# Kernel tuning notes

Measured on AMD Instinct MI355X. Metric: run time of the kernel, lower is better.

## Reference

```python
import jax, jax.numpy as jnp
import numpy as np

N = 50000      # nodes
E = 800000     # edges (no self-loops; conv adds them)
EMB = 64       # emb_dim
H = 4          # heads
C = EMB // H   # out_channels per head
L = 3          # num_layer
NEG = 0.2      # leaky_relu negative slope
EPS = 1e-5     # batchnorm eps


def setup_inputs() -> dict:
    key = jax.random.key(0)
    ks = jax.random.split(key, 12)
    x_idx = jax.random.randint(ks[0], (N,), 0, 16)
    src = jax.random.randint(ks[1], (E,), 0, N)
    off = jax.random.randint(ks[2], (E,), 1, N)
    dst = (src + off) % N  # guaranteed no self-loops
    edge_index = jnp.stack([src, dst])
    edge_attr_idx = jax.random.randint(ks[3], (E,), 0, 4)
    s = 0.1
    atom_emb = jax.random.normal(ks[4], (16, EMB)) * s
    W = jax.random.normal(ks[5], (L, EMB, H * C)) * s          # lin_src == lin_dst (shared)
    att_src = jax.random.normal(ks[6], (L, H, C)) * s
    att_dst = jax.random.normal(ks[7], (L, H, C)) * s
    att_edge = jax.random.normal(ks[8], (L, H, C)) * s
    bias = jnp.zeros((L, H * C))
    edge_emb = jax.random.normal(ks[9], (L, 4, H * C)) * s     # lin_edge embedding per layer
    bn_gamma = jnp.ones((L, EMB))
    bn_beta = jnp.zeros((L, EMB))
    pred_W = jax.random.normal(ks[10], (2 * EMB, 1)) * s
    pred_b = jnp.zeros((1,))
    return dict(x_idx=x_idx, edge_index=edge_index, edge_attr_idx=edge_attr_idx,
                atom_emb=atom_emb, W=W, att_src=att_src, att_dst=att_dst,
                att_edge=att_edge, bias=bias, edge_emb=edge_emb,
                bn_gamma=bn_gamma, bn_beta=bn_beta, pred_W=pred_W, pred_b=pred_b)


def _gat_forward(x_idx, edge_index, edge_attr_idx, atom_emb, W, att_src, att_dst,
                 att_edge, bias, edge_emb, bn_gamma, bn_beta, pred_W, pred_b):
    src, dst = edge_index[0], edge_index[1]
    loop = jnp.arange(N)
    src2 = jnp.concatenate([src, loop])   # edges + self-loops
    dst2 = jnp.concatenate([dst, loop])
    x = atom_emb[x_idx]                   # [N, EMB]
    for l in range(L):
        # embed edge attrs, self-loop fill = mean of incoming-edge features per node
        ea = edge_emb[l][edge_attr_idx]                                   # [E, H*C]
        cnt = jax.ops.segment_sum(jnp.ones((E,), ea.dtype), dst, N)       # [N]
        ea_mean = jax.ops.segment_sum(ea, dst, N) / jnp.clip(cnt, 1.0)[:, None]
        ea2 = jnp.concatenate([ea, ea_mean]).reshape(-1, H, C)            # [E+N, H, C]
        # shared src/dst projection
        xl = (x @ W[l]).reshape(N, H, C)                                  # [N, H, C]
        a_src = jnp.sum(xl * att_src[l], axis=-1)                         # [N, H]
        a_dst = jnp.sum(xl * att_dst[l], axis=-1)                         # [N, H]
        a_edge = jnp.sum(ea2 * att_edge[l], axis=-1)                      # [E+N, H]
        alpha = a_src[src2] + a_dst[dst2] + a_edge
        alpha = jnp.where(alpha >= 0, alpha, NEG * alpha)                 # leaky_relu
        # segment softmax over incoming edges of each destination node
        m = jax.ops.segment_max(alpha, dst2, N)                           # [N, H]
        ex = jnp.exp(alpha - m[dst2])
        denom = jax.ops.segment_sum(ex, dst2, N)
        alpha = ex / denom[dst2]                                          # [E+N, H]
        # message + scatter-add aggregate
        msg = alpha[:, :, None] * (xl[src2] + ea2)                        # [E+N, H, C]
        out = jax.ops.segment_sum(msg, dst2, N).reshape(N, H * C) + bias[l]
        # BatchNorm1d (training-mode batch stats, biased variance)
        mu = jnp.mean(out, axis=0)
        var = jnp.mean((out - mu) ** 2, axis=0)
        out = (out - mu) * jax.lax.rsqrt(var + EPS) * bn_gamma[l] + bn_beta[l]
        x = jax.nn.relu(out) + x                                          # residual
    pair = jnp.concatenate([x[src], x[dst]], axis=-1)                     # [E, 2*EMB]
    return pair @ pred_W + pred_b                                         # [E, 1]


def reference(x_idx, edge_index, edge_attr_idx, atom_emb, W, att_src, att_dst,
              att_edge, bias, edge_emb, bn_gamma, bn_beta, pred_W, pred_b):
    return _gat_forward(x_idx, edge_index, edge_attr_idx, atom_emb, W, att_src,
                        att_dst, att_edge, bias, edge_emb, bn_gamma, bn_beta,
                        pred_W, pred_b)
```

## Files before the change

kernel.cpp:

```cpp
#include <hip/hip_runtime.h>
#include <hip/hip_bf16.h>

#define NN 50000
#define NE 800000
#define NEG 0.2f
#define BNEPS 1e-5f
#define NB_CVT 61
#define NB_EDGE 3125
#define NB1 200
#define CH1 4000
#define NBKT 250
#define CAPBKT 4096
#define MAXS 288
#define NPARTS 32
#define NB_FRONT (NB_CVT + 1 + NB1)
#define NB_MID (NBKT + NN/16)

typedef __hip_bfloat16 bf16;
typedef unsigned short u16;
typedef unsigned int u32;
__device__ __forceinline__ float b2f(bf16 v){ return __bfloat162float(v); }
__device__ __forceinline__ float u2f(u16 u){ return __uint_as_float(((u32)u) << 16); }
__device__ __forceinline__ u16 f2u(float f){ bf16 b = __float2bfloat16(f); return *(u16*)&b; }

struct CvtArgs { const void* src[11]; int off[11]; int cnt[11]; };

__global__ __launch_bounds__(256) void k_front(CvtArgs a, const void* eeraw,
        const void* aeraw, const int* __restrict__ src, const int* __restrict__ dst,
        const int* __restrict__ ety,
        float* __restrict__ cw, float* __restrict__ aet, int* __restrict__ flag,
        int* __restrict__ bcur, u32* __restrict__ bins){
  int t = threadIdx.x, b = blockIdx.x;
  if (b >= NB_CVT + 1){
    __shared__ int cnt[NBKT], start[NBKT], cur[NBKT];
    __shared__ int dcache[CH1];
    int bb = b - (NB_CVT + 1);
    for (int i = t; i < NBKT; i += 256){ cnt[i] = 0; cur[i] = 0; }
    __syncthreads();
    int base = bb*CH1;
    for (int k = t; k < CH1; k += 256){
      int d = dst[base + k];
      dcache[k] = d;
      atomicAdd(&cnt[(u32)d/200u], 1);
    }
    __syncthreads();
    for (int i = t; i < NBKT; i += 256) start[i] = atomicAdd(&bcur[i], cnt[i]);
    __syncthreads();
    for (int k = t; k < CH1; k += 256){
      int e = base + k;
      u32 d = (u32)dcache[k];
      u32 bk = d/200u;
      int pos = start[bk] + atomicAdd(&cur[bk], 1);
      if (pos < CAPBKT)
        bins[bk*CAPBKT + pos] = (u32)src[e] | ((u32)ety[e] << 16) | ((d - bk*200u) << 18);
    }
    return;
  }
  __shared__ int sflag;
  if (t < 64){
    const u16* u = (const u16*)a.src[0];
    int hit = 0;
    for (int i = t; i < 512; i += 64){
      int ex = (u[i] >> 7) & 0xFF;
      if (ex >= 0x8A || (ex != 0 && ex <= 0x60)) hit = 1;
    }
    unsigned long long bl = __ballot(hit);
    if (t == 0) sflag = (bl != 0ULL) ? 1 : 0;
  }
  __syncthreads();
  int f = sflag;
  if (b == 0 && t == 0) *flag = f;
  if (b < NB_CVT){
    int i = b*256 + t;
    #pragma unroll
    for (int s = 0; s < 11; ++s){
      int j = i - a.off[s];
      if (j >= 0 && j < a.cnt[s])
        cw[a.off[s] + j] = f ? ((const float*)a.src[s])[j]
                             : b2f(((const bf16*)a.src[s])[j]);
    }
  } else if (t < 48){
    int l = t >> 4, ty = (t >> 2) & 3, h = t & 3;
    float s = 0.f;
    for (int cc = 0; cc < 16; ++cc){
      int ei = l*256 + ty*64 + h*16 + cc;
      int ai = l*64 + h*16 + cc;
      float ev = f ? ((const float*)eeraw)[ei] : b2f(((const bf16*)eeraw)[ei]);
      float av = f ? ((const float*)aeraw)[ai] : b2f(((const bf16*)aeraw)[ai]);
      s += ev*av;
    }
    aet[t] = s;
  }
}

__global__ __launch_bounds__(256) void k_mid(const int* __restrict__ bcur,
        const u32* __restrict__ bins,
        int* __restrict__ cpack, int* __restrict__ rowst, int* __restrict__ cnt4,
        const int* __restrict__ xidx, const float* __restrict__ aembf,
        const float* __restrict__ Wl, const float* __restrict__ att_s,
        const float* __restrict__ att_d,
        float* __restrict__ x, u16* __restrict__ bxl,
        float* __restrict__ asrc, float* __restrict__ adst){
  __shared__ __align__(16) char smem[17408];
  int t = threadIdx.x, b = blockIdx.x;
  if (b < NBKT){
    int* c4   = (int*)smem;
    int* nst  = c4 + 800;
    int* ncur = nst + 200;
    int* bco  = ncur + 200;
    int* s    = bco + 256;
    for (int i = t; i < 800; i += 256) c4[i] = 0;
    if (t < 200) ncur[t] = 0;
    int v = 0;
    if (t < NBKT){ v = bcur[t]; if (v > CAPBKT) v = CAPBKT; }
    bco[t] = v; s[t] = v;
    __syncthreads();
    for (int o = 1; o < 256; o <<= 1){
      int a2 = s[t]; int add = (t >= o) ? s[t-o] : 0;
      __syncthreads(); s[t] = a2 + add; __syncthreads();
    }
    int gb = s[b] - bco[b];
    int tot = bco[b];
    int total = s[255];
    __syncthreads();
    for (int i = t; i < tot; i += 256){
      u32 e = bins[b*CAPBKT + i];
      atomicAdd(&c4[((e >> 18) & 0xFF)*4 + ((e >> 16) & 3)], 1);
    }
    __syncthreads();
    int deg = 0;
    if (t < 200) deg = c4[t*4] + c4[t*4+1] + c4[t*4+2] + c4[t*4+3];
    s[t] = deg; __syncthreads();
    for (int o = 1; o < 256; o <<= 1){
      int a2 = s[t]; int add = (t >= o) ? s[t-o] : 0;
      __syncthreads(); s[t] = a2 + add; __syncthreads();
    }
    if (t < 200) nst[t] = s[t] - deg;
    __syncthreads();
    if (t < 200){
      int n = b*200 + t;
      rowst[n] = gb + nst[t];
      *(int4*)&cnt4[n*4] = make_int4(c4[t*4], c4[t*4+1], c4[t*4+2], c4[t*4+3]);
    }
    if (b == 0 && t == 0) rowst[NN] = total;
    for (int i = t; i < tot; i += 256){
      u32 e = bins[b*CAPBKT + i];
      int nl = (e >> 18) & 0xFF;
      int pos = nst[nl] + atomicAdd(&ncur[nl], 1);
      cpack[gb + pos] = (int)(e & 0x3FFFF);
    }
    return;
  }
  float* Ws = (float*)smem;
  float* xs = Ws + 4096;
  int bp = b - NBKT;
  for (int i = t; i < 4096; i += 256) Ws[i] = Wl[i];
  int c = t & 63, wv = t >> 6;
  float ats = att_s[c], atd = att_d[c];
  for (int pass = 0; pass < 4; ++pass){
    int n = bp*16 + pass*4 + wv;
    float xv = aembf[xidx[n]*64 + c];
    x[n*64 + c] = xv;
    __syncthreads();
    xs[t] = xv;
    __syncthreads();
    const float* xr = &xs[wv*64];
    float acc = 0.f;
    #pragma unroll
    for (int k = 0; k < 64; ++k) acc += xr[k]*Ws[k*64 + c];
    bxl[n*64 + c] = f2u(acc);
    float vs = acc*ats, vd = acc*atd;
    #pragma unroll
    for (int o = 8; o >= 1; o >>= 1){ vs += __shfl_xor(vs,o,64); vd += __shfl_xor(vd,o,64); }
    if ((c & 15) == 0){ asrc[n*4 + (c>>4)] = vs; adst[n*4 + (c>>4)] = vd; }
  }
}

__global__ __launch_bounds__(256) void k_bnproj(
    const float* __restrict__ opre, const float* __restrict__ bnp,
    const float* __restrict__ gam, const float* __restrict__ bet,
    const float* __restrict__ Wl,
    const float* __restrict__ att_s, const float* __restrict__ att_d,
    float* __restrict__ x, u16* __restrict__ bxl,
    float* __restrict__ asrc, float* __restrict__ adst){
  __shared__ float Ws[4096];
  __shared__ float xs[256];
  __shared__ float sred[256];
  __shared__ float stat[128];
  int t = threadIdx.x;
  {
    int cc = t & 127;
    float s = 0.f;
    for (int p2 = t >> 7; p2 < NPARTS; p2 += 2) s += bnp[p2*128 + cc];
    sred[t] = s;
  }
  for (int i = t; i < 4096; i += 256) Ws[i] = Wl[i];
  __syncthreads();
  if (t < 128) stat[t] = sred[t] + sred[128 + t];
  __syncthreads();
  int c = t & 63, wv = t >> 6;
  float mu  = stat[c] * (1.f/NN);
  float var = stat[64+c] * (1.f/NN) - mu*mu;
  float rstd = rsqrtf(var + BNEPS);
  float g = gam[c], be = bet[c];
  float ats = att_s[c], atd = att_d[c];
  for (int pass = 0; pass < 4; ++pass){
    int n = blockIdx.x*16 + pass*4 + wv;
    float o = (opre[n*64 + c] - mu)*rstd*g + be;
    float xv = x[n*64 + c] + fmaxf(o, 0.f);
    x[n*64 + c] = xv;
    __syncthreads();
    xs[t] = xv;
    __syncthreads();
    const float* xr = &xs[wv*64];
    float acc = 0.f;
    #pragma unroll
    for (int k = 0; k < 64; ++k) acc += xr[k]*Ws[k*64 + c];
    bxl[n*64 + c] = f2u(acc);
    float vs = acc*ats, vd = acc*atd;
    #pragma unroll
    for (int o2 = 8; o2 >= 1; o2 >>= 1){ vs += __shfl_xor(vs,o2,64); vd += __shfl_xor(vd,o2,64); }
    if ((c & 15) == 0){ asrc[n*4 + (c>>4)] = vs; adst[n*4 + (c>>4)] = vd; }
  }
}

__global__ __launch_bounds__(256) void k_aggr(
    const u16* __restrict__ bxl,
    const float* __restrict__ asrc, const float* __restrict__ adst,
    const int* __restrict__ cnt4, const int* __restrict__ rowst,
    const int* __restrict__ cpack,
    const float* __restrict__ eeg, const float* __restrict__ aetg,
    const float* __restrict__ biasg,
    float* __restrict__ opre, float* __restrict__ bnp){
  __shared__ __align__(16) float ee[256];
  __shared__ float aetL[16];
  __shared__ float adl[32];
  __shared__ float4 wsh[MAXS];
  __shared__ int ents[MAXS];
  __shared__ float redA[256], redB[256];
  __shared__ int rs[9];
  int t = threadIdx.x;
  int n0 = blockIdx.x*8;
  ee[t] = eeg[t];
  if (t < 16) aetL[t] = aetg[t];
  if (t >= 32 && t < 64) adl[t-32] = adst[n0*4 + (t-32)];
  if (t >= 64 && t < 73) rs[t-64] = rowst[n0 + (t-64)];
  __syncthreads();
  int jb0 = rs[0], je0 = rs[8], cnt = je0 - jb0;
  int lim = cnt < MAXS ? cnt : MAXS;
  for (int s = t; s < lim; s += 256){
    int j = jb0 + s;
    int pk = cpack[j];
    ents[s] = pk;
    int sr = pk & 0xFFFF, ty = pk >> 16;
    int dl = (j>=rs[1])+(j>=rs[2])+(j>=rs[3])+(j>=rs[4])+(j>=rs[5])+(j>=rs[6])+(j>=rs[7]);
    float4 as4 = *(const float4*)&asrc[sr*4];
    float a0 = as4.x + adl[dl*4+0] + aetL[ty*4+0]; a0 = a0>=0.f ? a0 : NEG*a0;
    float a1 = as4.y + adl[dl*4+1] + aetL[ty*4+1]; a1 = a1>=0.f ? a1 : NEG*a1;
    float a2 = as4.z + adl[dl*4+2] + aetL[ty*4+2]; a2 = a2>=0.f ? a2 : NEG*a2;
    float a3 = as4.w + adl[dl*4+3] + aetL[ty*4+3]; a3 = a3>=0.f ? a3 : NEG*a3;
    wsh[s] = make_float4(__expf(a0), __expf(a1), __expf(a2), __expf(a3));
  }
  __syncthreads();
  int wv = t >> 6, lane = t & 63;
  int ep = lane >> 5;
  int li = lane & 31;
  int ci = li << 1;
  int h = ci >> 4;
  const u32* bxl32 = (const u32*)bxl;
  const float* wshf = (const float*)wsh;
  float sA0 = 0.f, sA1 = 0.f, sB0 = 0.f, sB1 = 0.f;
  #pragma unroll
  for (int half = 0; half < 2; ++half){
    int node = wv + half*4;
    int n = n0 + node;
    int jb = rs[node], je = rs[node+1];
    int4 c4 = *(const int4*)&cnt4[n*4];
    int deg = c4.x + c4.y + c4.z + c4.w;
    float inv = 1.f / (float)(deg > 0 ? deg : 1);
    float2 eA = *(const float2*)&ee[ci];
    float2 eB = *(const float2*)&ee[64+ci];
    float2 eC = *(const float2*)&ee[128+ci];
    float2 eD = *(const float2*)&ee[192+ci];
    float eam0 = ((float)c4.x*eA.x + (float)c4.y*eB.x + (float)c4.z*eC.x + (float)c4.w*eD.x)*inv;
    float eam1 = ((float)c4.x*eA.y + (float)c4.y*eB.y + (float)c4.z*eC.y + (float)c4.w*eD.y)*inv;
    float aes = ((float)c4.x*aetL[h] + (float)c4.y*aetL[4+h]
               + (float)c4.z*aetL[8+h] + (float)c4.w*aetL[12+h]) * inv;
    float adn = adl[node*4 + h];
    float a = asrc[n*4 + h] + adn + aes;
    a = a >= 0.f ? a : NEG*a;
    float wself = __expf(a);
    u32 vs_ = bxl32[n*32 + li];
    float acc0, acc1, den;
    if (ep == 0){
      den = wself;
      acc0 = wself*(__uint_as_float(vs_ << 16) + eam0);
      acc1 = wself*(__uint_as_float(vs_ & 0xFFFF0000u) + eam1);
    } else { den = 0.f; acc0 = 0.f; acc1 = 0.f; }
    int jlim = jb0 + lim;
    int jeP = je < jlim ? je : jlim;
    int j = jb;
    for (; j + 8 <= jeP; j += 8){
      int so = j - jb0 + ep;
      int p0 = ents[so], p1 = ents[so+2], p2 = ents[so+4], p3 = ents[so+6];
      u32 v0 = bxl32[(p0 & 0xFFFF)*32 + li];
      u32 v1 = bxl32[(p1 & 0xFFFF)*32 + li];
      u32 v2 = bxl32[(p2 & 0xFFFF)*32 + li];
      u32 v3 = bxl32[(p3 & 0xFFFF)*32 + li];
      float w0 = wshf[(so  )*4 + h], w1 = wshf[(so+2)*4 + h];
      float w2 = wshf[(so+4)*4 + h], w3 = wshf[(so+6)*4 + h];
      float2 e0 = *(const float2*)&ee[(p0 >> 16)*64 + ci];
      float2 e1 = *(const float2*)&ee[(p1 >> 16)*64 + ci];
      float2 e2 = *(const float2*)&ee[(p2 >> 16)*64 + ci];
      float2 e3 = *(const float2*)&ee[(p3 >> 16)*64 + ci];
      acc0 += w0*(__uint_as_float(v0 << 16) + e0.x);
      acc1 += w0*(__uint_as_float(v0 & 0xFFFF0000u) + e0.y); den += w0;
      acc0 += w1*(__uint_as_float(v1 << 16) + e1.x);
      acc1 += w1*(__uint_as_float(v1 & 0xFFFF0000u) + e1.y); den += w1;
      acc0 += w2*(__uint_as_float(v2 << 16) + e2.x);
      acc1 += w2*(__uint_as_float(v2 & 0xFFFF0000u) + e2.y); den += w2;
      acc0 += w3*(__uint_as_float(v3 << 16) + e3.x);
      acc1 += w3*(__uint_as_float(v3 & 0xFFFF0000u) + e3.y); den += w3;
    }
    for (; j + 2 <= jeP; j += 2){
      int so = j - jb0 + ep;
      int p = ents[so];
      u32 v = bxl32[(p & 0xFFFF)*32 + li];
      float w = wshf[so*4 + h];
      float2 e = *(const float2*)&ee[(p >> 16)*64 + ci];
      acc0 += w*(__uint_as_float(v << 16) + e.x);
      acc1 += w*(__uint_as_float(v & 0xFFFF0000u) + e.y);
      den += w;
    }
    if (j < jeP && ep == 0){
      int so = j - jb0;
      int p = ents[so];
      u32 v = bxl32[(p & 0xFFFF)*32 + li];
      float w = wshf[so*4 + h];
      float2 e = *(const float2*)&ee[(p >> 16)*64 + ci];
      acc0 += w*(__uint_as_float(v << 16) + e.x);
      acc1 += w*(__uint_as_float(v & 0xFFFF0000u) + e.y);
      den += w;
    }
    for (j = jeP; j < je; ++j){
      if (ep == 0){
        int pk = cpack[j];
        int s_ = pk & 0xFFFF, ty = pk >> 16;
        float aa = asrc[s_*4 + h] + adn + aetL[ty*4 + h];
        aa = aa >= 0.f ? aa : NEG*aa;
        float wj = __expf(aa);
        u32 v = bxl32[s_*32 + li];
        float2 e = *(const float2*)&ee[ty*64 + ci];
        acc0 += wj*(__uint_as_float(v << 16) + e.x);
        acc1 += wj*(__uint_as_float(v & 0xFFFF0000u) + e.y);
        den += wj;
      }
    }
    acc0 += __shfl_xor(acc0, 32, 64);
    acc1 += __shfl_xor(acc1, 32, 64);
    den  += __shfl_xor(den, 32, 64);
    float2 bi = *(const float2*)&biasg[ci];
    float out0 = acc0/den + bi.x;
    float out1 = acc1/den + bi.y;
    if (ep == 0) *(float2*)&opre[n*64 + ci] = make_float2(out0, out1);
    sA0 += out0; sA1 += out1; sB0 += out0*out0; sB1 += out1*out1;
  }
  if (ep == 0){
    redA[wv*64 + ci] = sA0; redA[wv*64 + ci + 1] = sA1;
    redB[wv*64 + ci] = sB0; redB[wv*64 + ci + 1] = sB1;
  }
  __syncthreads();
  int part = blockIdx.x & (NPARTS-1);
  if (t < 64){
    atomicAdd(&bnp[part*128 + t], redA[t]+redA[64+t]+redA[128+t]+redA[192+t]);
  } else if (t < 128){
    int cc = t - 64;
    atomicAdd(&bnp[part*128 + 64 + cc], redB[cc]+redB[64+cc]+redB[128+cc]+redB[192+cc]);
  }
}

__global__ __launch_bounds__(256) void k_bnpred(
    const float* __restrict__ x, const float* __restrict__ opre,
    const float* __restrict__ bnp, const float* __restrict__ gam,
    const float* __restrict__ bet, const float* __restrict__ pW,
    float* __restrict__ s1, float* __restrict__ s2){
  __shared__ float sred[256];
  __shared__ float stat[128];
  int t = threadIdx.x;
  {
    int cc = t & 127;
    float s = 0.f;
    for (int p2 = t >> 7; p2 < NPARTS; p2 += 2) s += bnp[p2*128 + cc];
    sred[t] = s;
  }
  __syncthreads();
  if (t < 128) stat[t] = sred[t] + sred[128 + t];
  __syncthreads();
  int wv = t >> 6, c = t & 63;
  int n = blockIdx.x*4 + wv;
  float mu  = stat[c] * (1.f/NN);
  float var = stat[64+c] * (1.f/NN) - mu*mu;
  float o = (opre[n*64 + c] - mu)*rsqrtf(var + BNEPS)*gam[c] + bet[c];
  float xv = x[n*64 + c] + fmaxf(o, 0.f);
  float v1 = xv*pW[c], v2 = xv*pW[64 + c];
  #pragma unroll
  for (int o2 = 32; o2 >= 1; o2 >>= 1){ v1 += __shfl_xor(v1,o2,64); v2 += __shfl_xor(v2,o2,64); }
  if (c == 0){ s1[n] = v1; s2[n] = v2; }
}

__global__ void k_pred_edge(const int* __restrict__ src, const int* __restrict__ dst,
        const float* __restrict__ s1, const float* __restrict__ s2,
        const float* __restrict__ pbf, const int* __restrict__ flag, void* out){
  int e = blockIdx.x*256 + threadIdx.x;
  if (e < NE){
    float v = s1[src[e]] + s2[dst[e]] + pbf[0];
    if (*flag) ((float*)out)[e] = v;
    else       ((bf16*)out)[e] = __float2bfloat16(v);
  }
}

extern "C" void kernel_launch(void* const* d_in, const int* in_sizes, int n_in,
                              void* d_out, int out_size, void* d_ws, size_t ws_size,
                              hipStream_t stream){
  const int*  xidx = (const int*)d_in[0];
  const int*  eidx = (const int*)d_in[1];
  const int*  ety  = (const int*)d_in[2];
  const int* srcp = eidx, *dstp = eidx + NE;

  char* base = (char*)d_ws;
  auto alloc = [&](size_t bytes) -> char* {
    char* r = base; base += (bytes + 255) & ~(size_t)255; return r;
  };
  float* x      = (float*)alloc(NN*64*4);
  float* opre   = (float*)alloc(NN*64*4);
  float* asrc   = (float*)alloc(NN*4*4);
  float* adst   = (float*)alloc(NN*4*4);
  float* s1     = (float*)alloc(NN*4);
  float* s2     = (float*)alloc(NN*4);
  float* cw     = (float*)alloc(15392*4);
  float* aet    = (float*)alloc(64*4);
  char*  zchunk = alloc(3*NPARTS*128*4 + 256*4);
  float* bnpart = (float*)zchunk;
  int*   bcur   = (int*)(zchunk + 3*NPARTS*128*4);
  size_t zbytes = 3*NPARTS*128*4 + 256*4;
  u32*   bins   = (u32*)alloc((size_t)NBKT*CAPBKT*4);
  int*   cpack  = (int*)alloc(NE*4);
  int*   rowst  = (int*)alloc((NN+4)*4);
  int*   cnt4   = (int*)alloc(NN*4*4);
  int*   flag   = (int*)alloc(256);
  u16*   bxl    = (u16*)alloc(NN*64*2);

  const int O_AEMB = 0,     N_AEMB = 1024;
  const int O_W    = 1024,  N_W    = 12288;
  const int O_AS   = 13312, N_AS   = 192;
  const int O_AD   = 13504, N_AD   = 192;
  const int O_AE   = 13696, N_AE   = 192;
  const int O_BI   = 13888, N_BI   = 192;
  const int O_EE   = 14080, N_EE   = 768;
  const int O_GA   = 14848, N_GA   = 192;
  const int O_BE   = 15040, N_BE   = 192;
  const int O_PW   = 15232, N_PW   = 128;
  const int O_PB   = 15360, N_PB   = 1;

  CvtArgs ca;
  ca.src[0]=d_in[3];  ca.off[0]=O_AEMB; ca.cnt[0]=N_AEMB;
  ca.src[1]=d_in[4];  ca.off[1]=O_W;    ca.cnt[1]=N_W;
  ca.src[2]=d_in[5];  ca.off[2]=O_AS;   ca.cnt[2]=N_AS;
  ca.src[3]=d_in[6];  ca.off[3]=O_AD;   ca.cnt[3]=N_AD;
  ca.src[4]=d_in[7];  ca.off[4]=O_AE;   ca.cnt[4]=N_AE;
  ca.src[5]=d_in[8];  ca.off[5]=O_BI;   ca.cnt[5]=N_BI;
  ca.src[6]=d_in[9];  ca.off[6]=O_EE;   ca.cnt[6]=N_EE;
  ca.src[7]=d_in[10]; ca.off[7]=O_GA;   ca.cnt[7]=N_GA;
  ca.src[8]=d_in[11]; ca.off[8]=O_BE;   ca.cnt[8]=N_BE;
  ca.src[9]=d_in[12]; ca.off[9]=O_PW;   ca.cnt[9]=N_PW;
  ca.src[10]=d_in[13];ca.off[10]=O_PB;  ca.cnt[10]=N_PB;

  hipMemsetAsync(zchunk, 0, zbytes, stream);
  k_front<<<NB_FRONT, 256, 0, stream>>>(ca, d_in[9], d_in[7], srcp, dstp, ety,
                                        cw, aet, flag, bcur, bins);
  k_mid<<<NB_MID, 256, 0, stream>>>(bcur, bins, cpack, rowst, cnt4,
                                    xidx, cw + O_AEMB, cw + O_W,
                                    cw + O_AS, cw + O_AD, x, bxl, asrc, adst);
  for (int l = 0; l < 3; ++l){
    k_aggr<<<NN/8, 256, 0, stream>>>(bxl, asrc, adst, cnt4, rowst, cpack,
                                     cw + O_EE + l*256, aet + l*16,
                                     cw + O_BI + l*64, opre, bnpart + l*NPARTS*128);
    if (l < 2)
      k_bnproj<<<NN/16, 256, 0, stream>>>(opre, bnpart + l*NPARTS*128,
                                          cw + O_GA + l*64, cw + O_BE + l*64,
                                          cw + O_W + (l+1)*4096,
                                          cw + O_AS + (l+1)*64, cw + O_AD + (l+1)*64,
                                          x, bxl, asrc, adst);
  }
  k_bnpred<<<NN/4, 256, 0, stream>>>(x, opre, bnpart + 2*NPARTS*128,
                                     cw + O_GA + 128, cw + O_BE + 128,
                                     cw + O_PW, s1, s2);
  k_pred_edge<<<NB_EDGE, 256, 0, stream>>>(srcp, dstp, s1, s2, cw + O_PB, flag, d_out);
}
```

Before: 248.5 us.

## Factor edge-embedding term out of aggregation loop via per-type weight sums

The attention weights of the edges cached in shared memory are now accumulated per (destination node, edge type, head) with shared-memory atomics. Each node's edge-embedding contribution and softmax denominator are then formed once from these sums instead of per edge. The source index and a bf16-rounded weight are packed into one u32 per head, so the inner loop does one LDS load and drops the edge-embedding and denominator work. This cuts shared-memory traffic and ALU per edge, at the cost of bf16 rounding of the attention weights and extra LDS atomics in the setup phase.

```diff
diff --git a/kernel.cpp b/kernel.cpp
--- a/kernel.cpp
+++ b/kernel.cpp
@@ -235,8 +235,8 @@
   __shared__ __align__(16) float ee[256];
   __shared__ float aetL[16];
   __shared__ float adl[32];
-  __shared__ float4 wsh[MAXS];
-  __shared__ int ents[MAXS];
+  __shared__ u32 wsl[4*MAXS];
+  __shared__ float wsum[128];
   __shared__ float redA[256], redB[256];
   __shared__ int rs[9];
   int t = threadIdx.x;
@@ -245,13 +245,13 @@
   if (t < 16) aetL[t] = aetg[t];
   if (t >= 32 && t < 64) adl[t-32] = adst[n0*4 + (t-32)];
   if (t >= 64 && t < 73) rs[t-64] = rowst[n0 + (t-64)];
-  __syncthreads();
-  int jb0 = rs[0], je0 = rs[8], cnt = je0 - jb0;
+  if (t >= 128) wsum[t-128] = 0.f;
+  __syncthreads();
+  int jb0 = rs[0], cnt = rs[8] - jb0;
   int lim = cnt < MAXS ? cnt : MAXS;
   for (int s = t; s < lim; s += 256){
     int j = jb0 + s;
     int pk = cpack[j];
-    ents[s] = pk;
     int sr = pk & 0xFFFF, ty = pk >> 16;
     int dl = (j>=rs[1])+(j>=rs[2])+(j>=rs[3])+(j>=rs[4])+(j>=rs[5])+(j>=rs[6])+(j>=rs[7]);
     float4 as4 = *(const float4*)&asrc[sr*4];
@@ -259,16 +259,25 @@
     float a1 = as4.y + adl[dl*4+1] + aetL[ty*4+1]; a1 = a1>=0.f ? a1 : NEG*a1;
     float a2 = as4.z + adl[dl*4+2] + aetL[ty*4+2]; a2 = a2>=0.f ? a2 : NEG*a2;
     float a3 = as4.w + adl[dl*4+3] + aetL[ty*4+3]; a3 = a3>=0.f ? a3 : NEG*a3;
-    wsh[s] = make_float4(__expf(a0), __expf(a1), __expf(a2), __expf(a3));
+    u32 sr16 = (u32)sr << 16;
+    u16 b0 = f2u(__expf(a0)), b1 = f2u(__expf(a1));
+    u16 b2 = f2u(__expf(a2)), b3 = f2u(__expf(a3));
+    wsl[s]        = sr16 | b0;
+    wsl[MAXS+s]   = sr16 | b1;
+    wsl[2*MAXS+s] = sr16 | b2;
+    wsl[3*MAXS+s] = sr16 | b3;
+    int wb = dl*16 + ty*4;
+    atomicAdd(&wsum[wb+0], u2f(b0));
+    atomicAdd(&wsum[wb+1], u2f(b1));
+    atomicAdd(&wsum[wb+2], u2f(b2));
+    atomicAdd(&wsum[wb+3], u2f(b3));
   }
   __syncthreads();
   int wv = t >> 6, lane = t & 63;
-  int ep = lane >> 5;
-  int li = lane & 31;
-  int ci = li << 1;
-  int h = ci >> 4;
+  int ep = lane >> 5, li = lane & 31;
+  int ci = li << 1, h = ci >> 4;
   const u32* bxl32 = (const u32*)bxl;
-  const float* wshf = (const float*)wsh;
+  const u32* whp = &wsl[h*MAXS];
   float sA0 = 0.f, sA1 = 0.f, sB0 = 0.f, sB1 = 0.f;
   #pragma unroll
   for (int half = 0; half < 2; ++half){
@@ -282,67 +291,62 @@
     float2 eB = *(const float2*)&ee[64+ci];
     float2 eC = *(const float2*)&ee[128+ci];
     float2 eD = *(const float2*)&ee[192+ci];
-    float eam0 = ((float)c4.x*eA.x + (float)c4.y*eB.x + (float)c4.z*eC.x + (float)c4.w*eD.x)*inv;
-    float eam1 = ((float)c4.x*eA.y + (float)c4.y*eB.y + (float)c4.z*eC.y + (float)c4.w*eD.y)*inv;
     float aes = ((float)c4.x*aetL[h] + (float)c4.y*aetL[4+h]
                + (float)c4.z*aetL[8+h] + (float)c4.w*aetL[12+h]) * inv;
     float adn = adl[node*4 + h];
     float a = asrc[n*4 + h] + adn + aes;
     a = a >= 0.f ? a : NEG*a;
     float wself = __expf(a);
-    u32 vs_ = bxl32[n*32 + li];
-    float acc0, acc1, den;
+    float acc0 = 0.f, acc1 = 0.f, den = 0.f;
     if (ep == 0){
-      den = wself;
-      acc0 = wself*(__uint_as_float(vs_ << 16) + eam0);
-      acc1 = wself*(__uint_as_float(vs_ & 0xFFFF0000u) + eam1);
-    } else { den = 0.f; acc0 = 0.f; acc1 = 0.f; }
+      float eam0 = ((float)c4.x*eA.x + (float)c4.y*eB.x + (float)c4.z*eC.x + (float)c4.w*eD.x)*inv;
+      float eam1 = ((float)c4.x*eA.y + (float)c4.y*eB.y + (float)c4.z*eC.y + (float)c4.w*eD.y)*inv;
+      u32 vs_ = bxl32[n*32 + li];
+      float s0 = wsum[node*16 + h],     s1w = wsum[node*16 + 4 + h];
+      float s2w = wsum[node*16 + 8 + h], s3w = wsum[node*16 + 12 + h];
+      den = wself + s0 + s1w + s2w + s3w;
+      acc0 = wself*(__uint_as_float(vs_ << 16) + eam0)
+           + s0*eA.x + s1w*eB.x + s2w*eC.x + s3w*eD.x;
+      acc1 = wself*(__uint_as_float(vs_ & 0xFFFF0000u) + eam1)
+           + s0*eA.y + s1w*eB.y + s2w*eC.y + s3w*eD.y;
+    }
     int jlim = jb0 + lim;
     int jeP = je < jlim ? je : jlim;
     int j = jb;
     for (; j + 8 <= jeP; j += 8){
       int so = j - jb0 + ep;
-      int p0 = ents[so], p1 = ents[so+2], p2 = ents[so+4], p3 = ents[so+6];
-      u32 v0 = bxl32[(p0 & 0xFFFF)*32 + li];
-      u32 v1 = bxl32[(p1 & 0xFFFF)*32 + li];
-      u32 v2 = bxl32[(p2 & 0xFFFF)*32 + li];
-      u32 v3 = bxl32[(p3 & 0xFFFF)*32 + li];
-      float w0 = wshf[(so  )*4 + h], w1 = wshf[(so+2)*4 + h];
-      float w2 = wshf[(so+4)*4 + h], w3 = wshf[(so+6)*4 + h];
-      float2 e0 = *(const float2*)&ee[(p0 >> 16)*64 + ci];
-      float2 e1 = *(const float2*)&ee[(p1 >> 16)*64 + ci];
-      float2 e2 = *(const float2*)&ee[(p2 >> 16)*64 + ci];
-      float2 e3 = *(const float2*)&ee[(p3 >> 16)*64 + ci];
-      acc0 += w0*(__uint_as_float(v0 << 16) + e0.x);
-      acc1 += w0*(__uint_as_float(v0 & 0xFFFF0000u) + e0.y); den += w0;
-      acc0 += w1*(__uint_as_float(v1 << 16) + e1.x);
-      acc1 += w1*(__uint_as_float(v1 & 0xFFFF0000u) + e1.y); den += w1;
-      acc0 += w2*(__uint_as_float(v2 << 16) + e2.x);
-      acc1 += w2*(__uint_as_float(v2 & 0xFFFF0000u) + e2.y); den += w2;
-      acc0 += w3*(__uint_as_float(v3 << 16) + e3.x);
-      acc1 += w3*(__uint_as_float(v3 & 0xFFFF0000u) + e3.y); den += w3;
+      u32 p0 = whp[so],   p1 = whp[so+2], p2 = whp[so+4], p3 = whp[so+6];
+      u32 v0 = bxl32[(p0>>16)*32 + li], v1 = bxl32[(p1>>16)*32 + li];
+      u32 v2 = bxl32[(p2>>16)*32 + li], v3 = bxl32[(p3>>16)*32 + li];
+      float w0 = __uint_as_float(p0 << 16), w1 = __uint_as_float(p1 << 16);
+      float w2 = __uint_as_float(p2 << 16), w3 = __uint_as_float(p3 << 16);
+      acc0 += w0*__uint_as_float(v0 << 16);
+      acc1 += w0*__uint_as_float(v0 & 0xFFFF0000u);
+      acc0 += w1*__uint_as_float(v1 << 16);
+      acc1 += w1*__uint_as_float(v1 & 0xFFFF0000u);
+      acc0 += w2*__uint_as_float(v2 << 16);
+      acc1 += w2*__uint_as_float(v2 & 0xFFFF0000u);
+      acc0 += w3*__uint_as_float(v3 << 16);
+      acc1 += w3*__uint_as_float(v3 & 0xFFFF0000u);
     }
     for (; j + 2 <= jeP; j += 2){
       int so = j - jb0 + ep;
-      int p = ents[so];
-      u32 v = bxl32[(p & 0xFFFF)*32 + li];
-      float w = wshf[so*4 + h];
-      float2 e = *(const float2*)&ee[(p >> 16)*64 + ci];
-      acc0 += w*(__uint_as_float(v << 16) + e.x);
-      acc1 += w*(__uint_as_float(v & 0xFFFF0000u) + e.y);
-      den += w;
+      u32 p = whp[so];
+      u32 v = bxl32[(p>>16)*32 + li];
+      float w = __uint_as_float(p << 16);
+      acc0 += w*__uint_as_float(v << 16);
+      acc1 += w*__uint_as_float(v & 0xFFFF0000u);
     }
     if (j < jeP && ep == 0){
       int so = j - jb0;
-      int p = ents[so];
-      u32 v = bxl32[(p & 0xFFFF)*32 + li];
-      float w = wshf[so*4 + h];
-      float2 e = *(const float2*)&ee[(p >> 16)*64 + ci];
-      acc0 += w*(__uint_as_float(v << 16) + e.x);
-      acc1 += w*(__uint_as_float(v & 0xFFFF0000u) + e.y);
-      den += w;
-    }
-    for (j = jeP; j < je; ++j){
+      u32 p = whp[so];
+      u32 v = bxl32[(p>>16)*32 + li];
+      float w = __uint_as_float(p << 16);
+      acc0 += w*__uint_as_float(v << 16);
+      acc1 += w*__uint_as_float(v & 0xFFFF0000u);
+    }
+    int jf = jeP > jb ? jeP : jb;
+    for (j = jf; j < je; ++j){
       if (ep == 0){
         int pk = cpack[j];
         int s_ = pk & 0xFFFF, ty = pk >> 16;
@@ -358,12 +362,13 @@
     }
     acc0 += __shfl_xor(acc0, 32, 64);
     acc1 += __shfl_xor(acc1, 32, 64);
-    den  += __shfl_xor(den, 32, 64);
-    float2 bi = *(const float2*)&biasg[ci];
-    float out0 = acc0/den + bi.x;
-    float out1 = acc1/den + bi.y;
-    if (ep == 0) *(float2*)&opre[n*64 + ci] = make_float2(out0, out1);
-    sA0 += out0; sA1 += out1; sB0 += out0*out0; sB1 += out1*out1;
+    if (ep == 0){
+      float2 bi = *(const float2*)&biasg[ci];
+      float out0 = acc0/den + bi.x;
+      float out1 = acc1/den + bi.y;
+      *(float2*)&opre[n*64 + ci] = make_float2(out0, out1);
+      sA0 += out0; sA1 += out1; sB0 += out0*out0; sB1 += out1*out1;
+    }
   }
   if (ep == 0){
     redA[wv*64 + ci] = sA0; redA[wv*64 + ci + 1] = sA1;
```

Measured after the change: 284.4 us. 1.14x slower.
